# Kernel tuning notes

Measured on AMD Instinct MI355X. Metric: run time of the kernel, lower is better.

## Reference

```python
import jax, jax.numpy as jnp
import numpy as np

S, D, E = 16384, 4096, 64
CAPACITY_FACTOR = 1.25  # training mode
CAPACITY = int(CAPACITY_FACTOR * S / E)  # 320


def setup_inputs() -> dict:
    key = jax.random.key(0)
    kx, kw = jax.random.split(key)
    x = jax.random.normal(kx, (S, D), dtype=jnp.float32)
    W_g = jax.random.normal(kw, (E, D), dtype=jnp.float32) * (1.0 / np.sqrt(D))
    return {"x": x, "W_g": W_g}


def reference(x, W_g):
    # Router GEMM + softmax.  x: [S, D], W_g: [E, D] (nn.Linear weight layout).
    S_ = x.shape[0]
    E_ = W_g.shape[0]
    logits = x @ W_g.T                       # [S, E]
    gates = jax.nn.softmax(logits, axis=-1)  # [S, E]

    # Top-2 experts per token (topk is constant across the original per-token loop,
    # so we compute it once).
    vals, idx = jax.lax.top_k(gates, 2)
    g1, g2 = vals[:, 0], vals[:, 1]          # [S]
    e1, e2 = idx[:, 0], idx[:, 1]            # [S] int32
    denom = g1 + g2
    g1n = g1 / denom                         # normalized top-1 gate
    g2n = g2 / denom                         # normalized top-2 gate

    # Pass 1: top-1 dispatch, capacity-limited, serialized in token order.
    # cumsum of one-hot gives each token its 1-indexed position within its expert.
    m1 = jax.nn.one_hot(e1, E_, dtype=gates.dtype)              # [S, E]
    pos1 = jnp.sum(jnp.cumsum(m1, axis=0) * m1, axis=-1)        # [S]
    keep1 = pos1 <= CAPACITY                                    # [S] bool
    counts1 = jnp.sum(m1 * keep1[:, None].astype(gates.dtype), axis=0)  # [E]

    # Pass 2: top-2 dispatch with random keep prob (rnd < 2*g2n), capacity-limited
    # against the counts remaining after pass 1, again serialized in token order.
    rnd = jax.random.uniform(jax.random.key(1), (S_,), dtype=gates.dtype)
    want2 = rnd < 2.0 * g2n                                     # [S] bool
    m2 = jax.nn.one_hot(e2, E_, dtype=gates.dtype) * want2[:, None].astype(gates.dtype)
    pos2 = jnp.sum(jnp.cumsum(m2, axis=0) * m2, axis=-1)        # [S]
    keep2 = want2 & (pos2 <= (CAPACITY - counts1)[e2])          # [S] bool

    rows = jnp.arange(S_)
    combine = jnp.zeros_like(gates)
    combine = combine.at[rows, e1].set(jnp.where(keep1, g1n, 0.0))
    combine = combine.at[rows, e2].set(jnp.where(keep2, g2n, 0.0))
    return combine
```

## Files before the change

### kernel.cpp

```cpp
#include <hip/hip_runtime.h>
#include <stdint.h>

#define S 16384
#define D 4096
#define NE 64
#define CAP 320
#define WQ 4
#define KCH (D / WQ)
#define KSTEPS (KCH / 16)
#define NKS (D / 16)
#define K2ROWS 128
#define NB (S / K2ROWS)

typedef _Float16 f16x8 __attribute__((ext_vector_type(8)));
typedef float f32x16 __attribute__((ext_vector_type(16)));

__device__ __forceinline__ uint32_t rotl32(uint32_t v, int n) {
  return (v << n) | (v >> (32 - n));
}

__device__ uint32_t threefry_bits(int i) {
  const uint32_t k0 = 0u, k1 = 1u;
  const uint32_t ks2 = k0 ^ k1 ^ 0x1BD11BDAu;
  uint32_t x0 = 0u + k0;
  uint32_t x1 = (uint32_t)i + k1;
#define TFR(R) { x0 += x1; x1 = rotl32(x1, R); x1 ^= x0; }
  TFR(13) TFR(15) TFR(26) TFR(6)
  x0 += k1;  x1 += ks2 + 1u;
  TFR(17) TFR(29) TFR(16) TFR(24)
  x0 += ks2; x1 += k0 + 2u;
  TFR(13) TFR(15) TFR(26) TFR(6)
  x0 += k0;  x1 += k1 + 3u;
  TFR(17) TFR(29) TFR(16) TFR(24)
  x0 += k1;  x1 += ks2 + 4u;
  TFR(13) TFR(15) TFR(26) TFR(6)
  x0 += ks2; x1 += k0 + 5u;
#undef TFR
  return x0 ^ x1;
}

__global__ __launch_bounds__(256) void k0_packw(const float* __restrict__ Wg,
                                                f16x8* __restrict__ WH,
                                                f16x8* __restrict__ WL) {
  const int tid = blockIdx.x * 256 + threadIdx.x;
  const int lane = tid & 63;
  const int t = (tid >> 6) & 1;
  const int ks = tid >> 7;
  const int col = 32 * t + (lane & 31);
  const int k0 = ks * 16 + 8 * (lane >> 5);
  const float* wp = Wg + (size_t)col * D + k0;
  f16x8 h, l;
#pragma unroll
  for (int j = 0; j < 8; ++j) {
    const float w = wp[j];
    const _Float16 wh = (_Float16)w;
    const float r = (w - (float)wh) * 4096.0f;
    h[j] = wh;
    l[j] = (_Float16)r;
  }
  WH[tid] = h;
  WL[tid] = l;
}

__global__ __launch_bounds__(256) void k1_fused(const float* __restrict__ x,
                                                const f16x8* __restrict__ WH,
                                                const f16x8* __restrict__ WL,
                                                int* __restrict__ E1, int* __restrict__ E2,
                                                int* __restrict__ WANT,
                                                float* __restrict__ G1, float* __restrict__ G2) {
  __shared__ float lsum[WQ][32][64];
  const int w = threadIdx.x >> 6;
  const int lane = threadIdx.x & 63;
  const int rowBase = blockIdx.x * 32;
  const int row = rowBase + (lane & 31);
  const float* xp = x + (size_t)row * D + w * KCH + (lane >> 5) * 8;
  const int ks0 = w * KSTEPS;

  f32x16 acc0[2], acc1[2];
#pragma unroll
  for (int t = 0; t < 2; ++t)
#pragma unroll
    for (int r = 0; r < 16; ++r) { acc0[t][r] = 0.0f; acc1[t][r] = 0.0f; }

  float4 a0 = *(const float4*)(xp);
  float4 a1 = *(const float4*)(xp + 4);
#pragma unroll 2
  for (int s = 0; s < KSTEPS; ++s) {
    const int sn = (s + 1 < KSTEPS) ? s + 1 : s;
    const float4 a0n = *(const float4*)(xp + sn * 16);
    const float4 a1n = *(const float4*)(xp + sn * 16 + 4);
    const size_t fi = (size_t)(ks0 + s) * 128 + lane;
    const f16x8 bh0 = WH[fi];
    const f16x8 bh1 = WH[fi + 64];
    const f16x8 bl0 = WL[fi];
    const f16x8 bl1 = WL[fi + 64];

    const float af[8] = {a0.x, a0.y, a0.z, a0.w, a1.x, a1.y, a1.z, a1.w};
    f16x8 ah, al;
#pragma unroll
    for (int j = 0; j < 8; ++j) {
      const _Float16 h = (_Float16)af[j];
      ah[j] = h;
      al[j] = (_Float16)((af[j] - (float)h) * 4096.0f);
    }

    acc0[0] = __builtin_amdgcn_mfma_f32_32x32x16_f16(ah, bh0, acc0[0], 0, 0, 0);
    acc1[0] = __builtin_amdgcn_mfma_f32_32x32x16_f16(al, bh0, acc1[0], 0, 0, 0);
    acc1[0] = __builtin_amdgcn_mfma_f32_32x32x16_f16(ah, bl0, acc1[0], 0, 0, 0);
    acc0[1] = __builtin_amdgcn_mfma_f32_32x32x16_f16(ah, bh1, acc0[1], 0, 0, 0);
    acc1[1] = __builtin_amdgcn_mfma_f32_32x32x16_f16(al, bh1, acc1[1], 0, 0, 0);
    acc1[1] = __builtin_amdgcn_mfma_f32_32x32x16_f16(ah, bl1, acc1[1], 0, 0, 0);

    a0 = a0n; a1 = a1n;
  }

#pragma unroll
  for (int t = 0; t < 2; ++t) {
    const int col = 32 * t + (lane & 31);
#pragma unroll
    for (int r = 0; r < 16; ++r) {
      const int lrow = (r & 3) + 8 * (r >> 2) + 4 * (lane >> 5);
      lsum[w][lrow][col] = acc0[t][r] + acc1[t][r] * (1.0f / 4096.0f);
    }
  }
  __syncthreads();

  {
    float* p0 = &lsum[0][0][0];
    const float* p1 = &lsum[1][0][0];
    const float* p2 = &lsum[2][0][0];
    const float* p3 = &lsum[3][0][0];
#pragma unroll
    for (int j = 0; j < 8; ++j) {
      const int idx = threadIdx.x + 256 * j;
      p0[idx] = ((p0[idx] + p1[idx]) + p2[idx]) + p3[idx];
    }
  }
  __syncthreads();

  for (int rr = 0; rr < 8; ++rr) {
    const int lrow = w * 8 + rr;
    const int grow = rowBase + lrow;
    const float l = lsum[0][lrow][lane];

    float m = l;
#pragma unroll
    for (int off = 32; off; off >>= 1) m = fmaxf(m, __shfl_xor(m, off));
    const float ex = expf(l - m);
    float ssum = ex;
#pragma unroll
    for (int off = 32; off; off >>= 1) ssum += __shfl_xor(ssum, off);
    ssum = __shfl(ssum, 0);
    const float gate = ex / ssum;

    float v = gate; int id = lane;
#pragma unroll
    for (int off = 32; off; off >>= 1) {
      float vo = __shfl_xor(v, off); int io = __shfl_xor(id, off);
      if (vo > v || (vo == v && io < id)) { v = vo; id = io; }
    }
    const float g1 = v; const int e1 = id;
    const float gate2 = (lane == e1) ? -1.0f : gate;
    v = gate2; id = lane;
#pragma unroll
    for (int off = 32; off; off >>= 1) {
      float vo = __shfl_xor(v, off); int io = __shfl_xor(id, off);
      if (vo > v || (vo == v && io < id)) { v = vo; id = io; }
    }
    const float g2 = v; const int e2 = id;

    if (lane == 0) {
      const float denom = g1 + g2;
      const float g1n = g1 / denom;
      const float g2n = g2 / denom;
      const uint32_t bits = threefry_bits(grow);
      const float rnd = __uint_as_float((bits >> 9) | 0x3f800000u) - 1.0f;
      E1[grow] = e1; E2[grow] = e2;
      WANT[grow] = (rnd < 2.0f * g2n) ? 1 : 0;
      G1[grow] = g1n; G2[grow] = g2n;
    }
  }
}

__global__ __launch_bounds__(K2ROWS) void k2_rank(const int* __restrict__ E1,
                                                  const int* __restrict__ E2,
                                                  const int* __restrict__ WANT,
                                                  int* __restrict__ LR1, int* __restrict__ LR2,
                                                  int* __restrict__ H1, int* __restrict__ H2) {
  __shared__ unsigned char s1[K2ROWS], s2[K2ROWS];
  __shared__ int h1[NE], h2[NE];
  const int b = blockIdx.x, t = threadIdx.x;
  const int r = b * K2ROWS + t;
  if (t < NE) { h1[t] = 0; h2[t] = 0; }
  const int e1 = E1[r];
  const int e2 = WANT[r] ? E2[r] : NE;
  s1[t] = (unsigned char)e1;
  s2[t] = (unsigned char)e2;
  __syncthreads();
  int r1 = 0, r2 = 0;
  for (int j = 0; j < t; ++j) {
    r1 += (s1[j] == e1);
    r2 += (s2[j] == e2);
  }
  LR1[r] = r1; LR2[r] = r2;
  atomicAdd(&h1[e1], 1);
  if (e2 < NE) atomicAdd(&h2[e2], 1);
  __syncthreads();
  if (t < NE) { H1[b * NE + t] = h1[t]; H2[b * NE + t] = h2[t]; }
}

__global__ void k3_prefix(const int* __restrict__ H1, const int* __restrict__ H2,
                          int* __restrict__ OFF1, int* __restrict__ OFF2,
                          int* __restrict__ REM2) {
  const int e = threadIdx.x;
  int run1 = 0, run2 = 0;
  for (int b = 0; b < NB; ++b) {
    OFF1[b * NE + e] = run1; run1 += H1[b * NE + e];
    OFF2[b * NE + e] = run2; run2 += H2[b * NE + e];
  }
  REM2[e] = CAP - min(run1, CAP);
}

__global__ __launch_bounds__(256) void k4_scatter(const int* __restrict__ E1,
                                                  const int* __restrict__ E2,
                                                  const int* __restrict__ WANT,
                                                  const float* __restrict__ G1,
                                                  const float* __restrict__ G2,
                                                  const int* __restrict__ LR1,
                                                  const int* __restrict__ LR2,
                                                  const int* __restrict__ OFF1,
                                                  const int* __restrict__ OFF2,
                                                  const int* __restrict__ REM2,
                                                  float* __restrict__ out) {
  const int r = blockIdx.x * 256 + threadIdx.x;
  const int b = r / K2ROWS;
  const int e1 = E1[r];
  const int pos1 = OFF1[b * NE + e1] + LR1[r] + 1;
  if (pos1 <= CAP) out[(size_t)r * NE + e1] = G1[r];
  if (WANT[r]) {
    const int e2 = E2[r];
    const int pos2 = OFF2[b * NE + e2] + LR2[r] + 1;
    if (pos2 <= REM2[e2]) out[(size_t)r * NE + e2] = G2[r];
  }
}

extern "C" void kernel_launch(void* const* d_in, const int* in_sizes, int n_in,
                              void* d_out, int out_size, void* d_ws, size_t ws_size,
                              hipStream_t stream) {
  const float* x  = (const float*)d_in[0];
  const float* Wg = (const float*)d_in[1];
  float* out = (float*)d_out;
  char* ws = (char*)d_ws;

  size_t off = 0;
  int*   E1   = (int*)(ws + off);   off += (size_t)S * 4;
  int*   E2   = (int*)(ws + off);   off += (size_t)S * 4;
  int*   WANT = (int*)(ws + off);   off += (size_t)S * 4;
  float* G1   = (float*)(ws + off); off += (size_t)S * 4;
  float* G2   = (float*)(ws + off); off += (size_t)S * 4;
  int*   LR1  = (int*)(ws + off);   off += (size_t)S * 4;
  int*   LR2  = (int*)(ws + off);   off += (size_t)S * 4;
  int*   H1   = (int*)(ws + off);   off += (size_t)NB * NE * 4;
  int*   H2   = (int*)(ws + off);   off += (size_t)NB * NE * 4;
  int*   OFF1 = (int*)(ws + off);   off += (size_t)NB * NE * 4;
  int*   OFF2 = (int*)(ws + off);   off += (size_t)NB * NE * 4;
  int*   REM2 = (int*)(ws + off);   off += (size_t)NE * 4;
  f16x8* WH   = (f16x8*)(ws + off); off += (size_t)NKS * 2 * 64 * sizeof(f16x8);
  f16x8* WL   = (f16x8*)(ws + off); off += (size_t)NKS * 2 * 64 * sizeof(f16x8);

  hipMemsetAsync(d_out, 0, (size_t)out_size * sizeof(float), stream);
  k0_packw<<<128, 256, 0, stream>>>(Wg, WH, WL);
  k1_fused<<<S / 32, 256, 0, stream>>>(x, WH, WL, E1, E2, WANT, G1, G2);
  k2_rank<<<NB, K2ROWS, 0, stream>>>(E1, E2, WANT, LR1, LR2, H1, H2);
  k3_prefix<<<1, NE, 0, stream>>>(H1, H2, OFF1, OFF2, REM2);
  k4_scatter<<<S / 256, 256, 0, stream>>>(E1, E2, WANT, G1, G2, LR1, LR2, OFF1, OFF2, REM2, out);
}
```

Measured before the change: 416.6 us.

## Deepen GEMM prefetch pipeline, stage prefix in LDS, fuse output zeroing into write

The router GEMM loop now keeps three steps of x loads and two steps of packed weight loads in flight through a register ring, and sets launch bounds to target two blocks per CU. The prefix kernel first copies the block histograms into shared memory with 256 threads before the serial scan. The scatter kernel becomes a dense writer in which each wave writes full 64-wide output rows, zeros included, so the separate memset of the output is dropped. These target GEMM load latency, serial global reads in the scan, and one extra full pass over the output, at the cost of more registers held in the GEMM loop.

```diff
diff --git a/kernel.cpp b/kernel.cpp
--- a/kernel.cpp
+++ b/kernel.cpp
@@ -62,12 +62,15 @@
   WL[tid] = l;
 }
 
-__global__ __launch_bounds__(256) void k1_fused(const float* __restrict__ x,
-                                                const f16x8* __restrict__ WH,
-                                                const f16x8* __restrict__ WL,
-                                                int* __restrict__ E1, int* __restrict__ E2,
-                                                int* __restrict__ WANT,
-                                                float* __restrict__ G1, float* __restrict__ G2) {
+struct XS { float4 a, b; };
+struct BS { f16x8 h0, h1, l0, l1; };
+
+__global__ __launch_bounds__(256, 2) void k1_fused(const float* __restrict__ x,
+                                                   const f16x8* __restrict__ WH,
+                                                   const f16x8* __restrict__ WL,
+                                                   int* __restrict__ E1, int* __restrict__ E2,
+                                                   int* __restrict__ WANT,
+                                                   float* __restrict__ G1, float* __restrict__ G2) {
   __shared__ float lsum[WQ][32][64];
   const int w = threadIdx.x >> 6;
   const int lane = threadIdx.x & 63;
@@ -82,20 +85,30 @@
 #pragma unroll
     for (int r = 0; r < 16; ++r) { acc0[t][r] = 0.0f; acc1[t][r] = 0.0f; }
 
-  float4 a0 = *(const float4*)(xp);
-  float4 a1 = *(const float4*)(xp + 4);
-#pragma unroll 2
-  for (int s = 0; s < KSTEPS; ++s) {
-    const int sn = (s + 1 < KSTEPS) ? s + 1 : s;
-    const float4 a0n = *(const float4*)(xp + sn * 16);
-    const float4 a1n = *(const float4*)(xp + sn * 16 + 4);
+  auto LDX = [&](int s) {
+    XS r;
+    r.a = *(const float4*)(xp + s * 16);
+    r.b = *(const float4*)(xp + s * 16 + 4);
+    return r;
+  };
+  auto LDB = [&](int s) {
     const size_t fi = (size_t)(ks0 + s) * 128 + lane;
-    const f16x8 bh0 = WH[fi];
-    const f16x8 bh1 = WH[fi + 64];
-    const f16x8 bl0 = WL[fi];
-    const f16x8 bl1 = WL[fi + 64];
-
-    const float af[8] = {a0.x, a0.y, a0.z, a0.w, a1.x, a1.y, a1.z, a1.w};
+    BS r;
+    r.h0 = WH[fi];
+    r.h1 = WH[fi + 64];
+    r.l0 = WL[fi];
+    r.l1 = WL[fi + 64];
+    return r;
+  };
+
+  XS X0 = LDX(0), X1 = LDX(1), X2 = LDX(2);
+  BS B0 = LDB(0), B1 = LDB(1);
+
+  auto body = [&](int xs, int bs) {
+    XS Xn = LDX(xs);
+    BS Bn = LDB(bs);
+    const float af[8] = {X0.a.x, X0.a.y, X0.a.z, X0.a.w,
+                         X0.b.x, X0.b.y, X0.b.z, X0.b.w};
     f16x8 ah, al;
 #pragma unroll
     for (int j = 0; j < 8; ++j) {
@@ -103,16 +116,21 @@
       ah[j] = h;
       al[j] = (_Float16)((af[j] - (float)h) * 4096.0f);
     }
-
-    acc0[0] = __builtin_amdgcn_mfma_f32_32x32x16_f16(ah, bh0, acc0[0], 0, 0, 0);
-    acc1[0] = __builtin_amdgcn_mfma_f32_32x32x16_f16(al, bh0, acc1[0], 0, 0, 0);
-    acc1[0] = __builtin_amdgcn_mfma_f32_32x32x16_f16(ah, bl0, acc1[0], 0, 0, 0);
-    acc0[1] = __builtin_amdgcn_mfma_f32_32x32x16_f16(ah, bh1, acc0[1], 0, 0, 0);
-    acc1[1] = __builtin_amdgcn_mfma_f32_32x32x16_f16(al, bh1, acc1[1], 0, 0, 0);
-    acc1[1] = __builtin_amdgcn_mfma_f32_32x32x16_f16(ah, bl1, acc1[1], 0, 0, 0);
-
-    a0 = a0n; a1 = a1n;
-  }
+    acc0[0] = __builtin_amdgcn_mfma_f32_32x32x16_f16(ah, B0.h0, acc0[0], 0, 0, 0);
+    acc1[0] = __builtin_amdgcn_mfma_f32_32x32x16_f16(al, B0.h0, acc1[0], 0, 0, 0);
+    acc1[0] = __builtin_amdgcn_mfma_f32_32x32x16_f16(ah, B0.l0, acc1[0], 0, 0, 0);
+    acc0[1] = __builtin_amdgcn_mfma_f32_32x32x16_f16(ah, B0.h1, acc0[1], 0, 0, 0);
+    acc1[1] = __builtin_amdgcn_mfma_f32_32x32x16_f16(al, B0.h1, acc1[1], 0, 0, 0);
+    acc1[1] = __builtin_amdgcn_mfma_f32_32x32x16_f16(ah, B0.l1, acc1[1], 0, 0, 0);
+    X0 = X1; X1 = X2; X2 = Xn;
+    B0 = B1; B1 = Bn;
+  };
+
+#pragma unroll 4
+  for (int s = 0; s < KSTEPS - 3; ++s) body(s + 3, s + 2);
+  body(KSTEPS - 1, KSTEPS - 1);
+  body(KSTEPS - 1, KSTEPS - 1);
+  body(KSTEPS - 1, KSTEPS - 1);
 
 #pragma unroll
   for (int t = 0; t < 2; ++t) {
@@ -209,38 +227,56 @@
   if (t < NE) { H1[b * NE + t] = h1[t]; H2[b * NE + t] = h2[t]; }
 }
 
-__global__ void k3_prefix(const int* __restrict__ H1, const int* __restrict__ H2,
-                          int* __restrict__ OFF1, int* __restrict__ OFF2,
-                          int* __restrict__ REM2) {
-  const int e = threadIdx.x;
-  int run1 = 0, run2 = 0;
-  for (int b = 0; b < NB; ++b) {
-    OFF1[b * NE + e] = run1; run1 += H1[b * NE + e];
-    OFF2[b * NE + e] = run2; run2 += H2[b * NE + e];
-  }
-  REM2[e] = CAP - min(run1, CAP);
-}
-
-__global__ __launch_bounds__(256) void k4_scatter(const int* __restrict__ E1,
-                                                  const int* __restrict__ E2,
-                                                  const int* __restrict__ WANT,
-                                                  const float* __restrict__ G1,
-                                                  const float* __restrict__ G2,
-                                                  const int* __restrict__ LR1,
-                                                  const int* __restrict__ LR2,
-                                                  const int* __restrict__ OFF1,
-                                                  const int* __restrict__ OFF2,
-                                                  const int* __restrict__ REM2,
-                                                  float* __restrict__ out) {
-  const int r = blockIdx.x * 256 + threadIdx.x;
-  const int b = r / K2ROWS;
-  const int e1 = E1[r];
-  const int pos1 = OFF1[b * NE + e1] + LR1[r] + 1;
-  if (pos1 <= CAP) out[(size_t)r * NE + e1] = G1[r];
-  if (WANT[r]) {
-    const int e2 = E2[r];
-    const int pos2 = OFF2[b * NE + e2] + LR2[r] + 1;
-    if (pos2 <= REM2[e2]) out[(size_t)r * NE + e2] = G2[r];
+__global__ __launch_bounds__(256) void k3_prefix(const int* __restrict__ H1,
+                                                 const int* __restrict__ H2,
+                                                 int* __restrict__ OFF1, int* __restrict__ OFF2,
+                                                 int* __restrict__ REM2) {
+  __shared__ int sh1[NB * NE], sh2[NB * NE];
+  const int t = threadIdx.x;
+#pragma unroll
+  for (int j = 0; j < 8; ++j) {
+    const int i4 = t + 256 * j;
+    ((int4*)sh1)[i4] = ((const int4*)H1)[i4];
+    ((int4*)sh2)[i4] = ((const int4*)H2)[i4];
+  }
+  __syncthreads();
+  if (t < NE) {
+    int run1 = 0, run2 = 0;
+    for (int b = 0; b < NB; ++b) {
+      OFF1[b * NE + t] = run1; run1 += sh1[b * NE + t];
+      OFF2[b * NE + t] = run2; run2 += sh2[b * NE + t];
+    }
+    REM2[t] = CAP - min(run1, CAP);
+  }
+}
+
+__global__ __launch_bounds__(256) void k4_write(const int* __restrict__ E1,
+                                                const int* __restrict__ E2,
+                                                const int* __restrict__ WANT,
+                                                const float* __restrict__ G1,
+                                                const float* __restrict__ G2,
+                                                const int* __restrict__ LR1,
+                                                const int* __restrict__ LR2,
+                                                const int* __restrict__ OFF1,
+                                                const int* __restrict__ OFF2,
+                                                const int* __restrict__ REM2,
+                                                float* __restrict__ out) {
+  const int w = threadIdx.x >> 6, lane = threadIdx.x & 63;
+  const int rowBase = blockIdx.x * 16 + w * 4;
+#pragma unroll
+  for (int i = 0; i < 4; ++i) {
+    const int r = rowBase + i;
+    const int b = r / K2ROWS;
+    const int e1 = E1[r];
+    const int pos1 = OFF1[b * NE + e1] + LR1[r] + 1;
+    float val = 0.0f;
+    if (lane == e1 && pos1 <= CAP) val = G1[r];
+    if (WANT[r]) {
+      const int e2 = E2[r];
+      const int pos2 = OFF2[b * NE + e2] + LR2[r] + 1;
+      if (lane == e2 && pos2 <= REM2[e2]) val = G2[r];
+    }
+    out[(size_t)r * NE + lane] = val;
   }
 }
 
@@ -268,10 +304,9 @@
   f16x8* WH   = (f16x8*)(ws + off); off += (size_t)NKS * 2 * 64 * sizeof(f16x8);
   f16x8* WL   = (f16x8*)(ws + off); off += (size_t)NKS * 2 * 64 * sizeof(f16x8);
 
-  hipMemsetAsync(d_out, 0, (size_t)out_size * sizeof(float), stream);
   k0_packw<<<128, 256, 0, stream>>>(Wg, WH, WL);
   k1_fused<<<S / 32, 256, 0, stream>>>(x, WH, WL, E1, E2, WANT, G1, G2);
   k2_rank<<<NB, K2ROWS, 0, stream>>>(E1, E2, WANT, LR1, LR2, H1, H2);
-  k3_prefix<<<1, NE, 0, stream>>>(H1, H2, OFF1, OFF2, REM2);
-  k4_scatter<<<S / 256, 256, 0, stream>>>(E1, E2, WANT, G1, G2, LR1, LR2, OFF1, OFF2, REM2, out);
-}
+  k3_prefix<<<1, 256, 0, stream>>>(H1, H2, OFF1, OFF2, REM2);
+  k4_write<<<S / 16, 256, 0, stream>>>(E1, E2, WANT, G1, G2, LR1, LR2, OFF1, OFF2, REM2, out);
+}
```

Result: slower. 477.8 us (+14.7%).

## Split GEMM K across 8 waves, stage prefix histograms in LDS, fuse output zeroing

Applied to the files above, without the earlier changes.

The router GEMM kernel now splits the K dimension across 8 waves with 512-thread blocks instead of 4 waves, which adds parallelism per block at the cost of a larger LDS reduction. The prefix kernel bulk-loads both histograms into shared memory with vector loads before the serial per-expert scan. The scatter kernel is replaced by a dense writer where each wave writes full 64-wide output rows, zeros included, so the separate memset of the output goes away.

```diff
diff --git a/kernel.cpp b/kernel.cpp
--- a/kernel.cpp
+++ b/kernel.cpp
@@ -5,7 +5,7 @@
 #define D 4096
 #define NE 64
 #define CAP 320
-#define WQ 4
+#define WQ 8
 #define KCH (D / WQ)
 #define KSTEPS (KCH / 16)
 #define NKS (D / 16)
@@ -62,12 +62,12 @@
   WL[tid] = l;
 }
 
-__global__ __launch_bounds__(256) void k1_fused(const float* __restrict__ x,
-                                                const f16x8* __restrict__ WH,
-                                                const f16x8* __restrict__ WL,
-                                                int* __restrict__ E1, int* __restrict__ E2,
-                                                int* __restrict__ WANT,
-                                                float* __restrict__ G1, float* __restrict__ G2) {
+__global__ __launch_bounds__(512, 4) void k1_fused(const float* __restrict__ x,
+                                                   const f16x8* __restrict__ WH,
+                                                   const f16x8* __restrict__ WL,
+                                                   int* __restrict__ E1, int* __restrict__ E2,
+                                                   int* __restrict__ WANT,
+                                                   float* __restrict__ G1, float* __restrict__ G2) {
   __shared__ float lsum[WQ][32][64];
   const int w = threadIdx.x >> 6;
   const int lane = threadIdx.x & 63;
@@ -127,19 +127,19 @@
 
   {
     float* p0 = &lsum[0][0][0];
-    const float* p1 = &lsum[1][0][0];
-    const float* p2 = &lsum[2][0][0];
-    const float* p3 = &lsum[3][0][0];
-#pragma unroll
-    for (int j = 0; j < 8; ++j) {
-      const int idx = threadIdx.x + 256 * j;
-      p0[idx] = ((p0[idx] + p1[idx]) + p2[idx]) + p3[idx];
-    }
-  }
-  __syncthreads();
-
-  for (int rr = 0; rr < 8; ++rr) {
-    const int lrow = w * 8 + rr;
+#pragma unroll
+    for (int j = 0; j < 4; ++j) {
+      const int idx = threadIdx.x + 512 * j;
+      float v = p0[idx];
+#pragma unroll
+      for (int q = 1; q < WQ; ++q) v += (&lsum[0][0][0])[q * 2048 + idx];
+      p0[idx] = v;
+    }
+  }
+  __syncthreads();
+
+  for (int rr = 0; rr < 4; ++rr) {
+    const int lrow = w * 4 + rr;
     const int grow = rowBase + lrow;
     const float l = lsum[0][lrow][lane];
 
@@ -209,38 +209,56 @@
   if (t < NE) { H1[b * NE + t] = h1[t]; H2[b * NE + t] = h2[t]; }
 }
 
-__global__ void k3_prefix(const int* __restrict__ H1, const int* __restrict__ H2,
-                          int* __restrict__ OFF1, int* __restrict__ OFF2,
-                          int* __restrict__ REM2) {
-  const int e = threadIdx.x;
-  int run1 = 0, run2 = 0;
-  for (int b = 0; b < NB; ++b) {
-    OFF1[b * NE + e] = run1; run1 += H1[b * NE + e];
-    OFF2[b * NE + e] = run2; run2 += H2[b * NE + e];
-  }
-  REM2[e] = CAP - min(run1, CAP);
-}
-
-__global__ __launch_bounds__(256) void k4_scatter(const int* __restrict__ E1,
-                                                  const int* __restrict__ E2,
-                                                  const int* __restrict__ WANT,
-                                                  const float* __restrict__ G1,
-                                                  const float* __restrict__ G2,
-                                                  const int* __restrict__ LR1,
-                                                  const int* __restrict__ LR2,
-                                                  const int* __restrict__ OFF1,
-                                                  const int* __restrict__ OFF2,
-                                                  const int* __restrict__ REM2,
-                                                  float* __restrict__ out) {
-  const int r = blockIdx.x * 256 + threadIdx.x;
-  const int b = r / K2ROWS;
-  const int e1 = E1[r];
-  const int pos1 = OFF1[b * NE + e1] + LR1[r] + 1;
-  if (pos1 <= CAP) out[(size_t)r * NE + e1] = G1[r];
-  if (WANT[r]) {
-    const int e2 = E2[r];
-    const int pos2 = OFF2[b * NE + e2] + LR2[r] + 1;
-    if (pos2 <= REM2[e2]) out[(size_t)r * NE + e2] = G2[r];
+__global__ __launch_bounds__(256) void k3_prefix(const int* __restrict__ H1,
+                                                 const int* __restrict__ H2,
+                                                 int* __restrict__ OFF1, int* __restrict__ OFF2,
+                                                 int* __restrict__ REM2) {
+  __shared__ int sh1[NB * NE], sh2[NB * NE];
+  const int t = threadIdx.x;
+#pragma unroll
+  for (int j = 0; j < 8; ++j) {
+    const int i4 = t + 256 * j;
+    ((int4*)sh1)[i4] = ((const int4*)H1)[i4];
+    ((int4*)sh2)[i4] = ((const int4*)H2)[i4];
+  }
+  __syncthreads();
+  if (t < NE) {
+    int run1 = 0, run2 = 0;
+    for (int b = 0; b < NB; ++b) {
+      OFF1[b * NE + t] = run1; run1 += sh1[b * NE + t];
+      OFF2[b * NE + t] = run2; run2 += sh2[b * NE + t];
+    }
+    REM2[t] = CAP - min(run1, CAP);
+  }
+}
+
+__global__ __launch_bounds__(256) void k4_write(const int* __restrict__ E1,
+                                                const int* __restrict__ E2,
+                                                const int* __restrict__ WANT,
+                                                const float* __restrict__ G1,
+                                                const float* __restrict__ G2,
+                                                const int* __restrict__ LR1,
+                                                const int* __restrict__ LR2,
+                                                const int* __restrict__ OFF1,
+                                                const int* __restrict__ OFF2,
+                                                const int* __restrict__ REM2,
+                                                float* __restrict__ out) {
+  const int w = threadIdx.x >> 6, lane = threadIdx.x & 63;
+  const int rowBase = blockIdx.x * 16 + w * 4;
+#pragma unroll
+  for (int i = 0; i < 4; ++i) {
+    const int r = rowBase + i;
+    const int b = r / K2ROWS;
+    const int e1 = E1[r];
+    const int pos1 = OFF1[b * NE + e1] + LR1[r] + 1;
+    float val = 0.0f;
+    if (lane == e1 && pos1 <= CAP) val = G1[r];
+    if (WANT[r]) {
+      const int e2 = E2[r];
+      const int pos2 = OFF2[b * NE + e2] + LR2[r] + 1;
+      if (lane == e2 && pos2 <= REM2[e2]) val = G2[r];
+    }
+    out[(size_t)r * NE + lane] = val;
   }
 }
 
@@ -268,10 +286,9 @@
   f16x8* WH   = (f16x8*)(ws + off); off += (size_t)NKS * 2 * 64 * sizeof(f16x8);
   f16x8* WL   = (f16x8*)(ws + off); off += (size_t)NKS * 2 * 64 * sizeof(f16x8);
 
-  hipMemsetAsync(d_out, 0, (size_t)out_size * sizeof(float), stream);
   k0_packw<<<128, 256, 0, stream>>>(Wg, WH, WL);
-  k1_fused<<<S / 32, 256, 0, stream>>>(x, WH, WL, E1, E2, WANT, G1, G2);
+  k1_fused<<<S / 32, 512, 0, stream>>>(x, WH, WL, E1, E2, WANT, G1, G2);
   k2_rank<<<NB, K2ROWS, 0, stream>>>(E1, E2, WANT, LR1, LR2, H1, H2);
-  k3_prefix<<<1, NE, 0, stream>>>(H1, H2, OFF1, OFF2, REM2);
-  k4_scatter<<<S / 256, 256, 0, stream>>>(E1, E2, WANT, G1, G2, LR1, LR2, OFF1, OFF2, REM2, out);
-}
+  k3_prefix<<<1, 256, 0, stream>>>(H1, H2, OFF1, OFF2, REM2);
+  k4_write<<<S / 16, 256, 0, stream>>>(E1, E2, WANT, G1, G2, LR1, LR2, OFF1, OFF2, REM2, out);
+}
```

Result: faster. 395.8 us (-5.0%).
